# Kernel tuning notes

Hardware: AMD Instinct MI355X
Metric: run time of the kernel (lower is better)

## Reference

```python
import jax, jax.numpy as jnp
import numpy as np

B, L, M = 32768, 128, 1024  # batch, latent_size, num_basis_function


def setup_inputs() -> dict:
    key = jax.random.key(0)
    k1, k2, k3 = jax.random.split(key, 3)
    u_lat = jax.random.normal(k1, (B, L), dtype=jnp.float32)
    centres = jax.random.normal(k2, (M, L), dtype=jnp.float32)      # RBF centres (torch init: N(0,1))
    log_sigmas = jnp.zeros((M,), dtype=jnp.float32)                  # RBF log bandwidths (torch init: 0)
    lin1_w = jax.random.normal(k3, (M,), dtype=jnp.float32) / np.float32(np.sqrt(M))  # Linear(M,1,bias=False)
    return {"u_lat": u_lat, "centres": centres, "log_sigmas": log_sigmas, "lin1_w": lin1_w}


def _V_batch(u, centres, log_sigmas, lin1_w):
    """Potential V(h) = ELU(w . multiquadric(||h-c||/sigma)) + 0.5*||h||^2, per row. Returns [B]."""
    u_sq = jnp.sum(u * u, axis=-1)                                   # [B]
    c_sq = jnp.sum(centres * centres, axis=-1)                       # [M]
    # ||h - c||^2 via norm expansion: avoids [B, M, L] intermediate
    sq_dist = jnp.maximum(u_sq[:, None] + c_sq[None, :] - 2.0 * (u @ centres.T), 0.0)  # [B, M]
    d = jnp.sqrt(sq_dist) / jnp.exp(log_sigmas)[None, :]             # [B, M]
    phi = jnp.sqrt(1.0 + d * d)                                      # multiquadric kernel
    e = jax.nn.elu(phi @ lin1_w)                                     # [B]
    return e + 0.5 * u_sq


def reference(u_lat, centres, log_sigmas, lin1_w):
    # LEBNN.forward: f_lat = dV/dh evaluated per sample (vmap(jacrev) in torch).
    # Each entry of _V_batch depends only on its own row of u_lat, so
    # grad of the summed potential gives the per-sample Jacobian rows exactly.
    grad_fn = jax.grad(lambda u: jnp.sum(_V_batch(u, centres, log_sigmas, lin1_w)))
    return grad_fn(u_lat)  # [B, L]
```

## Files before the change

kernel.cpp:

```cpp
#include <hip/hip_runtime.h>
#include <math.h>

#define B_N 32768
#define L_N 128
#define M_N 1024
#define NT 512
#define TB 64
#define TM 64
#define NCHUNK (M_N / TM)

typedef __bf16 v8bf __attribute__((ext_vector_type(8)));
typedef __bf16 v4bf __attribute__((ext_vector_type(4)));
typedef float  v4f  __attribute__((ext_vector_type(4)));

#define MFMA(a, b, c) __builtin_amdgcn_mfma_f32_16x16x32_bf16(a, b, c, 0, 0, 0)

#define US  136
#define CNS 136

__device__ inline v8bf pack8(float4 a, float4 b) {
    v8bf v;
    v[0] = (__bf16)a.x; v[1] = (__bf16)a.y; v[2] = (__bf16)a.z; v[3] = (__bf16)a.w;
    v[4] = (__bf16)b.x; v[5] = (__bf16)b.y; v[6] = (__bf16)b.z; v[7] = (__bf16)b.w;
    return v;
}

__global__ void lebnn_precompute(const float* __restrict__ centres,
                                 const float* __restrict__ log_sigmas,
                                 const float* __restrict__ lin_w,
                                 float4* __restrict__ cpack) {
    int m = blockIdx.x * blockDim.x + threadIdx.x;
    if (m >= M_N) return;
    const float4* row = (const float4*)(centres + (size_t)m * L_N);
    float s = 0.f;
#pragma unroll
    for (int i = 0; i < L_N / 4; ++i) {
        float4 v = row[i];
        s += v.x * v.x + v.y * v.y + v.z * v.z + v.w * v.w;
    }
    float4 p;
    p.x = s;
    p.y = expf(-2.f * log_sigmas[m]);
    p.z = lin_w[m];
    p.w = 0.f;
    cpack[m] = p;
}

__global__ void lebnn_transpose(const float* __restrict__ centres,
                                __bf16* __restrict__ cT) {
    __shared__ __bf16 tile[64 * 72];
    const int m0 = blockIdx.x * 64;
    const int l0 = blockIdx.y * 64;
    const int row = threadIdx.x >> 2;
    const int seg = threadIdx.x & 3;
    const float* src = centres + (size_t)(m0 + row) * L_N + l0 + seg * 16;
    float4 a0 = *(const float4*)(src);
    float4 a1 = *(const float4*)(src + 4);
    float4 a2 = *(const float4*)(src + 8);
    float4 a3 = *(const float4*)(src + 12);
    *(v8bf*)&tile[row * 72 + seg * 16]     = pack8(a0, a1);
    *(v8bf*)&tile[row * 72 + seg * 16 + 8] = pack8(a2, a3);
    __syncthreads();
    v8bf o0, o1;
#pragma unroll
    for (int i = 0; i < 8; ++i) o0[i] = tile[(seg * 16 + i) * 72 + row];
#pragma unroll
    for (int i = 0; i < 8; ++i) o1[i] = tile[(seg * 16 + 8 + i) * 72 + row];
    __bf16* dst = cT + (size_t)(l0 + row) * M_N + m0 + seg * 16;
    *(v8bf*)(dst)     = o0;
    *(v8bf*)(dst + 8) = o1;
}

__global__ __launch_bounds__(NT) void lebnn_phase1(
    const float* __restrict__ u, const float* __restrict__ centres,
    const float4* __restrict__ cpack, __bf16* __restrict__ qg,
    float* __restrict__ gg, float* __restrict__ rsg)
{
    __shared__ __bf16 u_bf[64 * US];
    __shared__ __bf16 c_n[64 * CNS];
    __shared__ float usq_s[64];
    __shared__ float upart[64 * 9];
    __shared__ float sred[288];
    __shared__ float rred[288];

    const int tid  = threadIdx.x;
    const int w    = tid >> 6;
    const int lane = tid & 63;
    const int l15  = lane & 15;
    const int l4   = lane >> 4;
    const int bh   = w >> 2;
    const int mq   = w & 3;
    const int b0   = blockIdx.x * TB;

    {
        int row = tid >> 3, seg = tid & 7;
        const float* up = u + (size_t)(b0 + row) * L_N + seg * 16;
        float4 a0 = *(const float4*)(up);
        float4 a1 = *(const float4*)(up + 4);
        float4 a2 = *(const float4*)(up + 8);
        float4 a3 = *(const float4*)(up + 12);
        float ps = a0.x*a0.x + a0.y*a0.y + a0.z*a0.z + a0.w*a0.w
                 + a1.x*a1.x + a1.y*a1.y + a1.z*a1.z + a1.w*a1.w
                 + a2.x*a2.x + a2.y*a2.y + a2.z*a2.z + a2.w*a2.w
                 + a3.x*a3.x + a3.y*a3.y + a3.z*a3.z + a3.w*a3.w;
        *(v8bf*)&u_bf[row * US + seg * 16]     = pack8(a0, a1);
        *(v8bf*)&u_bf[row * US + seg * 16 + 8] = pack8(a2, a3);
        upart[row * 9 + seg] = ps;
    }
    __syncthreads();
    if (tid < TB) {
        float s = 0.f;
#pragma unroll
        for (int i = 0; i < 8; ++i) s += upart[tid * 9 + i];
        usq_s[tid] = s;
    }
    __syncthreads();

    v8bf uf[2][4];
#pragma unroll
    for (int bt = 0; bt < 2; ++bt)
#pragma unroll
        for (int kk = 0; kk < 4; ++kk)
            uf[bt][kk] = *(v8bf*)&u_bf[(bh*32 + bt*16 + l15) * US + kk*32 + l4*8];

    float usq_r[2][4];
#pragma unroll
    for (int bt = 0; bt < 2; ++bt)
#pragma unroll
        for (int r = 0; r < 4; ++r)
            usq_r[bt][r] = usq_s[bh*32 + bt*16 + l4*4 + r];

    float s_p[2][4] = {{0.f,0.f,0.f,0.f},{0.f,0.f,0.f,0.f}};
    float r_p[2][4] = {{0.f,0.f,0.f,0.f},{0.f,0.f,0.f,0.f}};

    const int rp = tid >> 4;
    const int cg = tid & 15;

    for (int mt = 0; mt < NCHUNK; ++mt) {
        const int m0 = mt * TM;
        __syncthreads();
        {
            const float* cp0 = centres + (size_t)(m0 + 2*rp) * L_N + cg * 8;
            float4 r0a = *(const float4*)(cp0);
            float4 r0b = *(const float4*)(cp0 + 4);
            float4 r1a = *(const float4*)(cp0 + L_N);
            float4 r1b = *(const float4*)(cp0 + L_N + 4);
            *(v8bf*)&c_n[(2*rp)     * CNS + cg*8] = pack8(r0a, r0b);
            *(v8bf*)&c_n[(2*rp + 1) * CNS + cg*8] = pack8(r1a, r1b);
        }
        float4 cpv = cpack[m0 + mq*16 + l15];
        __syncthreads();

        v4f dot[2];
        dot[0] = (v4f){0.f,0.f,0.f,0.f};
        dot[1] = (v4f){0.f,0.f,0.f,0.f};
#pragma unroll
        for (int kk = 0; kk < 4; ++kk) {
            v8bf bfr = *(v8bf*)&c_n[(mq*16 + l15) * CNS + kk*32 + l4*8];
            dot[0] = MFMA(uf[0][kk], bfr, dot[0]);
            dot[1] = MFMA(uf[1][kk], bfr, dot[1]);
        }

#pragma unroll
        for (int bt = 0; bt < 2; ++bt) {
#pragma unroll
            for (int r = 0; r < 4; ++r) {
                float dv  = dot[bt][r];
                float raw = fmaf(-2.f, dv, usq_r[bt][r] + cpv.x);
                float x   = fmaf(fmaxf(raw, 0.f), cpv.y, 1.f);
                float ri  = rsqrtf(x);
                s_p[bt][r] = fmaf(cpv.z, x * ri, s_p[bt][r]);
                float qv  = (raw > 0.f) ? cpv.z * cpv.y * ri : 0.f;
                r_p[bt][r] += qv;
                qg[(size_t)(b0 + bh*32 + bt*16 + l4*4 + r) * M_N + m0 + mq*16 + l15]
                    = (__bf16)qv;
            }
        }
    }

#pragma unroll
    for (int bt = 0; bt < 2; ++bt)
#pragma unroll
        for (int r = 0; r < 4; ++r) {
#pragma unroll
            for (int msk = 1; msk < 16; msk <<= 1) {
                s_p[bt][r] += __shfl_xor(s_p[bt][r], msk, 64);
                r_p[bt][r] += __shfl_xor(r_p[bt][r], msk, 64);
            }
        }
    if (l15 == 0) {
#pragma unroll
        for (int bt = 0; bt < 2; ++bt)
#pragma unroll
            for (int r = 0; r < 4; ++r) {
                sred[w*36 + bt*16 + l4*4 + r] = s_p[bt][r];
                rred[w*36 + bt*16 + l4*4 + r] = r_p[bt][r];
            }
    }
    __syncthreads();

    if (tid < TB) {
        int bhh = tid >> 5, rowr = tid & 31;
        float s = 0.f, R = 0.f;
#pragma unroll
        for (int i = 0; i < 4; ++i) {
            s += sred[(bhh*4 + i)*36 + rowr];
            R += rred[(bhh*4 + i)*36 + rowr];
        }
        float g = (s > 0.f) ? 1.f : expf(s);
        gg[b0 + tid]  = g;
        rsg[b0 + tid] = fmaf(g, R, 1.f);
    }
}

__global__ __launch_bounds__(NT) void lebnn_gemm2(
    const __bf16* __restrict__ qg, const __bf16* __restrict__ cT,
    float* __restrict__ Tg)
{
    __shared__ __bf16 qt[64 * 72];
    __shared__ __bf16 ct[128 * 72];

    const int tid  = threadIdx.x;
    const int w    = tid >> 6;
    const int lane = tid & 63;
    const int l15  = lane & 15;
    const int l4   = lane >> 4;
    const int bh   = w >> 2;
    const int lq   = w & 3;
    const int bb0  = blockIdx.x * 64;

    v4f acc[2][2];
#pragma unroll
    for (int bt = 0; bt < 2; ++bt)
#pragma unroll
        for (int lt = 0; lt < 2; ++lt)
            acc[bt][lt] = (v4f){0.f, 0.f, 0.f, 0.f};

    for (int mt = 0; mt < NCHUNK; ++mt) {
        const int m0 = mt * TM;
        __syncthreads();
        {
            int row = tid >> 3, seg = tid & 7;
            *(v8bf*)&qt[row * 72 + seg * 8] =
                *(const v8bf*)(qg + (size_t)(bb0 + row) * M_N + m0 + seg * 8);
        }
        {
            int lr = tid >> 2, sg = tid & 3;
            const __bf16* src = cT + (size_t)lr * M_N + m0 + sg * 16;
            *(v8bf*)&ct[lr * 72 + sg * 16]     = *(const v8bf*)(src);
            *(v8bf*)&ct[lr * 72 + sg * 16 + 8] = *(const v8bf*)(src + 8);
        }
        __syncthreads();

#pragma unroll
        for (int kk = 0; kk < 2; ++kk) {
            v8bf qa0 = *(v8bf*)&qt[(bh*32 +  0 + l15) * 72 + kk*32 + l4*8];
            v8bf qa1 = *(v8bf*)&qt[(bh*32 + 16 + l15) * 72 + kk*32 + l4*8];
#pragma unroll
            for (int lt = 0; lt < 2; ++lt) {
                v8bf cb = *(v8bf*)&ct[(lq*32 + lt*16 + l15) * 72 + kk*32 + l4*8];
                acc[0][lt] = MFMA(qa0, cb, acc[0][lt]);
                acc[1][lt] = MFMA(qa1, cb, acc[1][lt]);
            }
        }
    }

#pragma unroll
    for (int bt = 0; bt < 2; ++bt)
#pragma unroll
        for (int lt = 0; lt < 2; ++lt)
#pragma unroll
            for (int r = 0; r < 4; ++r)
                Tg[(size_t)(bb0 + bh*32 + bt*16 + l4*4 + r) * L_N
                   + lq*32 + lt*16 + l15] = acc[bt][lt][r];
}

__global__ __launch_bounds__(256) void lebnn_epilogue(
    const float* __restrict__ u, const float* __restrict__ Tg,
    const float* __restrict__ gg, const float* __restrict__ rsg,
    float* __restrict__ out)
{
    int i = blockIdx.x * 256 + threadIdx.x;
    int b = i >> 5;
    float4 uu = ((const float4*)u)[i];
    float4 tt = ((const float4*)Tg)[i];
    float g = gg[b], rs = rsg[b];
    float4 o;
    o.x = fmaf(uu.x, rs, -g * tt.x);
    o.y = fmaf(uu.y, rs, -g * tt.y);
    o.z = fmaf(uu.z, rs, -g * tt.z);
    o.w = fmaf(uu.w, rs, -g * tt.w);
    ((float4*)out)[i] = o;
}

#define CFS 68
#define OFF_UBF   0
#define OFF_CN    17408
#define OFF_CFL   34816
#define OFF_USQ   52224
#define OFF_UPART 52480
#define OFF_SRED  54784
#define OFF_RRED  55936
#define OFF_G     57088
#define OFF_RS    57344
#define SMEM_BYTES 57600

__global__ __launch_bounds__(NT) void lebnn_fallback(
    const float* __restrict__ u, const float* __restrict__ centres,
    const float4* __restrict__ cpack, float* __restrict__ out)
{
    extern __shared__ char smem[];
    __bf16* u_bf = (__bf16*)(smem + OFF_UBF);
    __bf16* c_n  = (__bf16*)(smem + OFF_CN);
    float*  cfl  = (float*)(smem + OFF_CFL);
    float* usq_s = (float*)(smem + OFF_USQ);
    float* upart = (float*)(smem + OFF_UPART);
    float* sred  = (float*)(smem + OFF_SRED);
    float* rred  = (float*)(smem + OFF_RRED);
    float* gsh   = (float*)(smem + OFF_G);
    float* rssh  = (float*)(smem + OFF_RS);

    const int tid  = threadIdx.x;
    const int w    = tid >> 6;
    const int lane = tid & 63;
    const int l15  = lane & 15;
    const int l4   = lane >> 4;
    const int bh   = w >> 2;
    const int mq   = w & 3;
    const int tx   = tid & 15;
    const int ty   = tid >> 4;
    const int b0   = blockIdx.x * TB;

    {
        int row = tid >> 3, seg = tid & 7;
        const float* up = u + (size_t)(b0 + row) * L_N + seg * 16;
        float4 a0 = *(const float4*)(up);
        float4 a1 = *(const float4*)(up + 4);
        float4 a2 = *(const float4*)(up + 8);
        float4 a3 = *(const float4*)(up + 12);
        float ps = a0.x*a0.x + a0.y*a0.y + a0.z*a0.z + a0.w*a0.w
                 + a1.x*a1.x + a1.y*a1.y + a1.z*a1.z + a1.w*a1.w
                 + a2.x*a2.x + a2.y*a2.y + a2.z*a2.z + a2.w*a2.w
                 + a3.x*a3.x + a3.y*a3.y + a3.z*a3.z + a3.w*a3.w;
        *(v8bf*)&u_bf[row * US + seg * 16]     = pack8(a0, a1);
        *(v8bf*)&u_bf[row * US + seg * 16 + 8] = pack8(a2, a3);
        upart[row * 9 + seg] = ps;
    }
    __syncthreads();
    if (tid < TB) {
        float s = 0.f;
#pragma unroll
        for (int i = 0; i < 8; ++i) s += upart[tid * 9 + i];
        usq_s[tid] = s;
    }
    __syncthreads();

    v8bf uf[2][4];
#pragma unroll
    for (int bt = 0; bt < 2; ++bt)
#pragma unroll
        for (int kk = 0; kk < 4; ++kk)
            uf[bt][kk] = *(v8bf*)&u_bf[(bh*32 + bt*16 + l15) * US + kk*32 + l4*8];

    float usq_r[2][4];
#pragma unroll
    for (int bt = 0; bt < 2; ++bt)
#pragma unroll
        for (int r = 0; r < 4; ++r)
            usq_r[bt][r] = usq_s[bh*32 + bt*16 + l4*4 + r];

    float s_p[2][4] = {{0.f,0.f,0.f,0.f},{0.f,0.f,0.f,0.f}};
    float r_p[2][4] = {{0.f,0.f,0.f,0.f},{0.f,0.f,0.f,0.f}};
    float T[4][4] = {{0.f}};

    const int rp = tid >> 4;
    const int cg = tid & 15;

    for (int mt = 0; mt < NCHUNK; ++mt) {
        const int m0 = mt * TM;
        __syncthreads();
        {
            const float* cp0 = centres + (size_t)(m0 + 2*rp) * L_N + cg * 8;
            float4 r0a = *(const float4*)(cp0);
            float4 r0b = *(const float4*)(cp0 + 4);
            float4 r1a = *(const float4*)(cp0 + L_N);
            float4 r1b = *(const float4*)(cp0 + L_N + 4);
            *(v8bf*)&c_n[(2*rp)     * CNS + cg*8] = pack8(r0a, r0b);
            *(v8bf*)&c_n[(2*rp + 1) * CNS + cg*8] = pack8(r1a, r1b);
        }
        float4 cpv = cpack[m0 + mq*16 + l15];
        __syncthreads();

        v4f dot[2];
        dot[0] = (v4f){0.f,0.f,0.f,0.f};
        dot[1] = (v4f){0.f,0.f,0.f,0.f};
#pragma unroll
        for (int kk = 0; kk < 4; ++kk) {
            v8bf bfr = *(v8bf*)&c_n[(mq*16 + l15) * CNS + kk*32 + l4*8];
            dot[0] = MFMA(uf[0][kk], bfr, dot[0]);
            dot[1] = MFMA(uf[1][kk], bfr, dot[1]);
        }

#pragma unroll
        for (int bt = 0; bt < 2; ++bt) {
#pragma unroll
            for (int r = 0; r < 4; ++r) {
                float dv  = dot[bt][r];
                float raw = fmaf(-2.f, dv, usq_r[bt][r] + cpv.x);
                float x   = fmaf(fmaxf(raw, 0.f), cpv.y, 1.f);
                float ri  = rsqrtf(x);
                s_p[bt][r] = fmaf(cpv.z, x * ri, s_p[bt][r]);
                float qv  = (raw > 0.f) ? cpv.z * cpv.y * ri : 0.f;
                r_p[bt][r] += qv;
                cfl[(mq*16 + l15) * CFS + bh*32 + bt*16 + l4*4 + r] = qv;
            }
        }
        __syncthreads();

        for (int mm = 0; mm < TM; ++mm) {
            v4f cf = *(v4f*)&cfl[mm * CFS + tx*4];
            v4bf cb = *(v4bf*)&c_n[mm * CNS + ty*4];
            float cv[4] = {(float)cb[0], (float)cb[1], (float)cb[2], (float)cb[3]};
#pragma unroll
            for (int i = 0; i < 4; ++i)
#pragma unroll
                for (int j = 0; j < 4; ++j)
                    T[i][j] = fmaf(cf[i], cv[j], T[i][j]);
        }
    }

    __syncthreads();

#pragma unroll
    for (int bt = 0; bt < 2; ++bt)
#pragma unroll
        for (int r = 0; r < 4; ++r) {
#pragma unroll
            for (int msk = 1; msk < 16; msk <<= 1) {
                s_p[bt][r] += __shfl_xor(s_p[bt][r], msk, 64);
                r_p[bt][r] += __shfl_xor(r_p[bt][r], msk, 64);
            }
        }
    if (l15 == 0) {
#pragma unroll
        for (int bt = 0; bt < 2; ++bt)
#pragma unroll
            for (int r = 0; r < 4; ++r) {
                sred[w*36 + bt*16 + l4*4 + r] = s_p[bt][r];
                rred[w*36 + bt*16 + l4*4 + r] = r_p[bt][r];
            }
    }
    __syncthreads();

    if (tid < TB) {
        int bhh = tid >> 5, rowr = tid & 31;
        float s = 0.f, R = 0.f;
#pragma unroll
        for (int i = 0; i < 4; ++i) {
            s += sred[(bhh*4 + i)*36 + rowr];
            R += rred[(bhh*4 + i)*36 + rowr];
        }
        float g = (s > 0.f) ? 1.f : expf(s);
        gsh[tid]  = g;
        rssh[tid] = fmaf(g, R, 1.f);
    }
    __syncthreads();

#pragma unroll
    for (int i = 0; i < 4; ++i) {
        int b = tx*4 + i;
        float rv = rssh[b];
        float gv = gsh[b];
        size_t idx = (size_t)(b0 + b) * L_N + ty*4;
        float4 uu = *(const float4*)(u + idx);
        float4 o;
        o.x = fmaf(uu.x, rv, -gv * T[i][0]);
        o.y = fmaf(uu.y, rv, -gv * T[i][1]);
        o.z = fmaf(uu.z, rv, -gv * T[i][2]);
        o.w = fmaf(uu.w, rv, -gv * T[i][3]);
        *(float4*)(out + idx) = o;
    }
}

extern "C" void kernel_launch(void* const* d_in, const int* in_sizes, int n_in,
                              void* d_out, int out_size, void* d_ws, size_t ws_size,
                              hipStream_t stream) {
    const float* u          = (const float*)d_in[0];
    const float* centres    = (const float*)d_in[1];
    const float* log_sigmas = (const float*)d_in[2];
    const float* lin_w      = (const float*)d_in[3];
    float* out = (float*)d_out;

    char* wsb = (char*)d_ws;
    float4* cpack = (float4*)wsb;
    __bf16* cT    = (__bf16*)(wsb + 16384);
    float*  gg    = (float*) (wsb + 278528);
    float*  rsg   = (float*) (wsb + 409600);
    __bf16* qg    = (__bf16*)(wsb + 540672);
    float*  Tg    = out;
    const size_t WS_NEED = 540672ULL + 67108864ULL + 16777216ULL;
    Tg = (float*)(wsb + 540672 + 67108864);

    lebnn_precompute<<<(M_N + 255) / 256, 256, 0, stream>>>(centres, log_sigmas, lin_w, cpack);

    if (ws_size >= WS_NEED) {
        lebnn_transpose<<<dim3(M_N / 64, L_N / 64), 256, 0, stream>>>(centres, cT);
        lebnn_phase1<<<B_N / TB, NT, 0, stream>>>(u, centres, cpack, qg, gg, rsg);
        lebnn_gemm2<<<B_N / 64, NT, 0, stream>>>(qg, cT, Tg);
        lebnn_epilogue<<<(B_N * L_N / 4) / 256, 256, 0, stream>>>(u, Tg, gg, rsg, out);
    } else {
        hipFuncSetAttribute((const void*)lebnn_fallback,
                            hipFuncAttributeMaxDynamicSharedMemorySize, SMEM_BYTES);
        lebnn_fallback<<<B_N / TB, NT, SMEM_BYTES, stream>>>(u, centres, cpack, out);
    }
}
```

Baseline: 77.23 us.

## Store Q in MFMA-fragment tile order and fuse epilogue into second GEMM

Phase 1 now writes each thread's eight bf16 Q values as one contiguous 16-byte vector, laid out per block, chunk and thread, instead of scattered 2-byte stores into a row-major [B,M] matrix. The second GEMM reads that tiled layout and scatters it into shared memory in the matching order. The separate epilogue kernel is folded into the GEMM, which applies the u*rs - g*T combination directly. This removes the Tg intermediate round trip and one kernel launch, at the cost of scattered shared-memory writes and uncoalesced scalar output stores.

```diff
diff --git a/kernel.cpp b/kernel.cpp
--- a/kernel.cpp
+++ b/kernel.cpp
@@ -161,6 +161,8 @@
             dot[1] = MFMA(uf[1][kk], bfr, dot[1]);
         }
 
+        v8bf qv8;
+        const float wq = cpv.z * cpv.y;
 #pragma unroll
         for (int bt = 0; bt < 2; ++bt) {
 #pragma unroll
@@ -170,12 +172,12 @@
                 float x   = fmaf(fmaxf(raw, 0.f), cpv.y, 1.f);
                 float ri  = rsqrtf(x);
                 s_p[bt][r] = fmaf(cpv.z, x * ri, s_p[bt][r]);
-                float qv  = (raw > 0.f) ? cpv.z * cpv.y * ri : 0.f;
+                float qv  = (raw > 0.f) ? wq * ri : 0.f;
                 r_p[bt][r] += qv;
-                qg[(size_t)(b0 + bh*32 + bt*16 + l4*4 + r) * M_N + m0 + mq*16 + l15]
-                    = (__bf16)qv;
-            }
-        }
+                qv8[bt*4 + r] = (__bf16)qv;
+            }
+        }
+        *(v8bf*)(qg + ((size_t)blockIdx.x * NCHUNK + mt) * (NT * 8) + tid * 8) = qv8;
     }
 
 #pragma unroll
@@ -214,8 +216,9 @@
 }
 
 __global__ __launch_bounds__(NT) void lebnn_gemm2(
-    const __bf16* __restrict__ qg, const __bf16* __restrict__ cT,
-    float* __restrict__ Tg)
+    const float* __restrict__ u, const __bf16* __restrict__ qg,
+    const __bf16* __restrict__ cT, const float* __restrict__ gg,
+    const float* __restrict__ rsg, float* __restrict__ out)
 {
     __shared__ __bf16 qt[64 * 72];
     __shared__ __bf16 ct[128 * 72];
@@ -240,9 +243,12 @@
         const int m0 = mt * TM;
         __syncthreads();
         {
-            int row = tid >> 3, seg = tid & 7;
-            *(v8bf*)&qt[row * 72 + seg * 8] =
-                *(const v8bf*)(qg + (size_t)(bb0 + row) * M_N + m0 + seg * 8);
+            v8bf qv = *(const v8bf*)(qg + ((size_t)blockIdx.x * NCHUNK + mt) * (NT * 8) + tid * 8);
+#pragma unroll
+            for (int bt = 0; bt < 2; ++bt)
+#pragma unroll
+                for (int r = 0; r < 4; ++r)
+                    qt[(bh*32 + bt*16 + l4*4 + r) * 72 + lq*16 + l15] = qv[bt*4 + r];
         }
         {
             int lr = tid >> 2, sg = tid & 3;
@@ -265,32 +271,25 @@
         }
     }
 
+    float gv[2][4], rv[2][4];
+#pragma unroll
+    for (int bt = 0; bt < 2; ++bt)
+#pragma unroll
+        for (int r = 0; r < 4; ++r) {
+            int b = bb0 + bh*32 + bt*16 + l4*4 + r;
+            gv[bt][r] = gg[b];
+            rv[bt][r] = rsg[b];
+        }
 #pragma unroll
     for (int bt = 0; bt < 2; ++bt)
 #pragma unroll
         for (int lt = 0; lt < 2; ++lt)
 #pragma unroll
-            for (int r = 0; r < 4; ++r)
-                Tg[(size_t)(bb0 + bh*32 + bt*16 + l4*4 + r) * L_N
-                   + lq*32 + lt*16 + l15] = acc[bt][lt][r];
-}
-
-__global__ __launch_bounds__(256) void lebnn_epilogue(
-    const float* __restrict__ u, const float* __restrict__ Tg,
-    const float* __restrict__ gg, const float* __restrict__ rsg,
-    float* __restrict__ out)
-{
-    int i = blockIdx.x * 256 + threadIdx.x;
-    int b = i >> 5;
-    float4 uu = ((const float4*)u)[i];
-    float4 tt = ((const float4*)Tg)[i];
-    float g = gg[b], rs = rsg[b];
-    float4 o;
-    o.x = fmaf(uu.x, rs, -g * tt.x);
-    o.y = fmaf(uu.y, rs, -g * tt.y);
-    o.z = fmaf(uu.z, rs, -g * tt.z);
-    o.w = fmaf(uu.w, rs, -g * tt.w);
-    ((float4*)out)[i] = o;
+            for (int r = 0; r < 4; ++r) {
+                size_t idx = (size_t)(bb0 + bh*32 + bt*16 + l4*4 + r) * L_N
+                           + lq*32 + lt*16 + l15;
+                out[idx] = fmaf(u[idx], rv[bt][r], -gv[bt][r] * acc[bt][lt][r]);
+            }
 }
 
 #define CFS 68
@@ -497,17 +496,14 @@
     float*  gg    = (float*) (wsb + 278528);
     float*  rsg   = (float*) (wsb + 409600);
     __bf16* qg    = (__bf16*)(wsb + 540672);
-    float*  Tg    = out;
-    const size_t WS_NEED = 540672ULL + 67108864ULL + 16777216ULL;
-    Tg = (float*)(wsb + 540672 + 67108864);
+    const size_t WS_NEED = 540672ULL + 67108864ULL;
 
     lebnn_precompute<<<(M_N + 255) / 256, 256, 0, stream>>>(centres, log_sigmas, lin_w, cpack);
 
     if (ws_size >= WS_NEED) {
         lebnn_transpose<<<dim3(M_N / 64, L_N / 64), 256, 0, stream>>>(centres, cT);
         lebnn_phase1<<<B_N / TB, NT, 0, stream>>>(u, centres, cpack, qg, gg, rsg);
-        lebnn_gemm2<<<B_N / 64, NT, 0, stream>>>(qg, cT, Tg);
-        lebnn_epilogue<<<(B_N * L_N / 4) / 256, 256, 0, stream>>>(u, Tg, gg, rsg, out);
+        lebnn_gemm2<<<B_N / 64, NT, 0, stream>>>(u, qg, cT, gg, rsg, out);
     } else {
         hipFuncSetAttribute((const void*)lebnn_fallback,
                             hipFuncAttributeMaxDynamicSharedMemorySize, SMEM_BYTES);
```

Measured after the change: 73.07 us. -5.4%, faster.
